# Optimization experiments

Measured on AMD Instinct MI355X. Metric: run time of the kernel, lower is better.

The kernel has to match this reference:

```python
import jax, jax.numpy as jnp
import numpy as np

B, T, I, H, L, O = 2048, 512, 1, 64, 2, 1


def _lstm_layer(x, Wih, Whh, b):
    """Single LSTM layer, batch_first x: [B, T, in] -> [B, T, H].
    PyTorch gate order: i, f, g, o. b = b_ih + b_hh (folded)."""
    Bn = x.shape[0]
    Hn = Whh.shape[1]
    # Precompute input contribution for all timesteps (hoisted out of scan)
    xg = jnp.einsum('bti,gi->btg', x, Wih) + b  # [B, T, 4H]

    def step(carry, xg_t):
        h, c = carry
        g = xg_t + h @ Whh.T  # [B, 4H]
        i, f, gg, o = jnp.split(g, 4, axis=-1)
        i = jax.nn.sigmoid(i)
        f = jax.nn.sigmoid(f)
        gg = jnp.tanh(gg)
        o = jax.nn.sigmoid(o)
        c = f * c + i * gg
        h = o * jnp.tanh(c)
        return (h, c), h

    h0 = jnp.zeros((Bn, Hn), x.dtype)
    c0 = jnp.zeros((Bn, Hn), x.dtype)
    (_, _), hs = jax.lax.scan(step, (h0, c0), jnp.swapaxes(xg, 0, 1))  # hs: [T, B, H]
    return jnp.swapaxes(hs, 0, 1)


def setup_inputs() -> dict:
    key = jax.random.key(0)
    ks = jax.random.split(key, 11)
    s = 1.0 / np.sqrt(H)  # torch default uniform bound
    u = lambda k, shp: jax.random.uniform(k, shp, jnp.float32, -s, s)
    return {
        'x': jax.random.normal(ks[0], (B, T, I), jnp.float32),
        'Wih0': u(ks[1], (4 * H, I)),
        'Whh0': u(ks[2], (4 * H, H)),
        'bih0': u(ks[3], (4 * H,)),
        'bhh0': u(ks[4], (4 * H,)),
        'Wih1': u(ks[5], (4 * H, H)),
        'Whh1': u(ks[6], (4 * H, H)),
        'bih1': u(ks[7], (4 * H,)),
        'bhh1': u(ks[8], (4 * H,)),
        'fcW': u(ks[9], (O, H)),
        'fcb': u(ks[10], (O,)),
    }


def reference(x, Wih0, Whh0, bih0, bhh0, Wih1, Whh1, bih1, bhh1, fcW, fcb):
    h1 = _lstm_layer(x, Wih0, Whh0, bih0 + bhh0)   # [B, T, H]
    h2 = _lstm_layer(h1, Wih1, Whh1, bih1 + bhh1)  # [B, T, H]
    return h2[:, -1, :] @ fcW.T + fcb               # [B, O]
```

## Files before the change

kernel.cpp:

```cpp
#include <hip/hip_runtime.h>


#define TT 512
#define HH 64
#define BT 8

typedef __attribute__((ext_vector_type(4))) int i32x4;

#define MFMAI8 __builtin_amdgcn_mfma_i32_16x16x64_i8

#define WSCALE 260096.0f
#define HSCALE 32512.0f
#define LOG2E  1.44269504f
constexpr float C_SIG = (float)(256.0 / (260096.0 * 32512.0) * 1.4426950408889634);
constexpr float C_TGH = (float)(2.0 * 256.0 / (260096.0 * 32512.0) * 1.4426950408889634);

__device__ __forceinline__ float exp2_hw(float x) {
    float r; asm("v_exp_f32 %0, %1" : "=v"(r) : "v"(x)); return r;
}
__device__ __forceinline__ float exp2n_hw(float x) {
    float r; asm("v_exp_f32 %0, -%1" : "=v"(r) : "v"(x)); return r;
}
__device__ __forceinline__ float gate4s(float p0, float p1, float p2, float p3, float& c) {
    float gi = __builtin_amdgcn_rcpf(1.f + exp2n_hw(p0));
    float gf = __builtin_amdgcn_rcpf(1.f + exp2n_hw(p1));
    float gg = 1.f - 2.f * __builtin_amdgcn_rcpf(1.f + exp2_hw(p2));
    float go = __builtin_amdgcn_rcpf(1.f + exp2n_hw(p3));
    c = fmaf(gf, c, gi * gg);
    float tc = 1.f - 2.f * __builtin_amdgcn_rcpf(1.f + exp2_hw(c * (2.f * LOG2E)));
    return go * tc;
}
__device__ __forceinline__ int dpp_ror8_i(int v) {
    return __builtin_amdgcn_update_dpp(v, v, 0x128, 0xF, 0xF, true);
}
__device__ __forceinline__ void cvtW16(const float* __restrict__ p, i32x4& hi, i32x4& lo) {
    #pragma unroll
    for (int r = 0; r < 4; ++r) {
        int hw = 0, lw = 0;
        #pragma unroll
        for (int b = 0; b < 4; ++b) {
            int wq = (int)rintf(p[4 * b + r] * WSCALE);
            int h8 = (wq + 128) >> 8;
            int l8 = wq - (h8 << 8);
            hw |= (h8 & 0xFF) << (8 * b);
            lw |= (l8 & 0xFF) << (8 * b);
        }
        hi[r] = hw; lo[r] = lw;
    }
}

__global__ __launch_bounds__(1024) void lstm_mfma(
    const float* __restrict__ x,
    const float* __restrict__ Wih0, const float* __restrict__ Whh0,
    const float* __restrict__ bih0, const float* __restrict__ bhh0,
    const float* __restrict__ Wih1, const float* __restrict__ Whh1,
    const float* __restrict__ bih1, const float* __restrict__ bhh1,
    const float* __restrict__ fcW, const float* __restrict__ fcb,
    float* __restrict__ out)
{
    __shared__ float xs[BT][TT + 1];
    __shared__ __align__(16) signed char aH[2][2][2][64][16];
    __shared__ float hF[BT][HH + 1];
    __shared__ float fcw_s[HH];

    const int t    = threadIdx.x;
    const int lane = t & 63;
    const int w    = t >> 6;
    const int b0   = blockIdx.x * BT;
    const int m    = lane & 15;
    const int q    = lane >> 4;
    const int ts   = m >> 3;
    const int bpk  = m & 7;
    const int jpk  = 4 * w + q;

    for (int i = t; i < BT * TT; i += 1024)
        xs[i >> 9][i & (TT - 1)] = x[(size_t)(b0 + (i >> 9)) * TT + (i & (TT - 1))];
    {
        int* z = (int*)aH;
        for (int i = t; i < 2048; i += 1024)
            z[i] = ((i >> 8) & 1) ? 0x80808080 : 0;
    }
    if (t < HH) fcw_s[t] = fcW[t];

    i32x4 A0h, A0l, I1h, I1l, H1h, H1l;
    {
        const int rho = (m & 3) * 64 + 4 * w + (m >> 2);
        cvtW16(Whh0 + rho * HH + q * 16, A0h, A0l);
        cvtW16(Wih1 + rho * HH + q * 16, I1h, I1l);
        cvtW16(Whh1 + rho * HH + q * 16, H1h, H1l);
    }

    i32x4 corrA, corrB;
    {
        i32x4 ones; ones[0] = 0x01010101; ones[1] = 0x01010101;
        ones[2] = 0x01010101; ones[3] = 0x01010101;
        i32x4 zz = {0, 0, 0, 0};
        i32x4 Sa = MFMAI8(A0h, ones, zz, 0, 0, 0);
        i32x4 Sb = MFMAI8(I1h, ones, zz, 0, 0, 0);
        Sb = MFMAI8(H1h, ones, Sb, 0, 0, 0);
        #pragma unroll
        for (int r = 0; r < 4; ++r) { corrA[r] = Sa[r] << 7; corrB[r] = Sb[r] << 7; }
    }

    float wxb[4], bia[4];
    #pragma unroll
    for (int v = 0; v < 4; ++v) {
        const int r = v * 64 + jpk;
        const float sc = (v == 2) ? 2.f * LOG2E : LOG2E;
        if (ts) { wxb[v] = 0.f;          bia[v] = (bih1[r] + bhh1[r]) * sc; }
        else    { wxb[v] = Wih0[r] * sc; bia[v] = (bih0[r] + bhh0[r]) * sc; }
    }
    const int wl = ((jpk >> 4) << 4) + bpk;
    const int wb = ((jpk & 3) << 2) | ((jpk >> 2) & 3);
    float c = 0.f;

    __syncthreads();

    #pragma unroll 2
    for (int k = 0; k < TT; ++k) {
        const int p = k & 1, pn = p ^ 1;
        i32x4 bh1 = *(const i32x4*)&aH[0][p][0][lane][0];
        i32x4 bl1 = *(const i32x4*)&aH[0][p][1][lane][0];
        i32x4 bh2 = *(const i32x4*)&aH[1][p][0][lane][0];
        i32x4 bl2 = *(const i32x4*)&aH[1][p][1][lane][0];
        i32x4 z4 = {0, 0, 0, 0};
        i32x4 aHHr = z4, bHHr = z4;
        i32x4 aMDr = corrA, bMDr = corrB;
        aHHr = MFMAI8(A0h, bh1, aHHr, 0, 0, 0);
        bHHr = MFMAI8(I1h, bh1, bHHr, 0, 0, 0);
        aMDr = MFMAI8(A0h, bl1, aMDr, 0, 0, 0);
        bMDr = MFMAI8(I1h, bl1, bMDr, 0, 0, 0);
        aMDr = MFMAI8(A0l, bh1, aMDr, 0, 0, 0);
        bMDr = MFMAI8(I1l, bh1, bMDr, 0, 0, 0);
        bHHr = MFMAI8(H1h, bh2, bHHr, 0, 0, 0);
        bMDr = MFMAI8(H1h, bl2, bMDr, 0, 0, 0);
        bMDr = MFMAI8(H1l, bh2, bMDr, 0, 0, 0);

        float xb = xs[bpk][k];
        float pre[4];
        #pragma unroll
        for (int r = 0; r < 4; ++r) {
            int hh = aHHr[r] + dpp_ror8_i(bHHr[r]);
            int md = aMDr[r] + dpp_ror8_i(bMDr[r]);
            float P = (float)((hh << 8) + md);
            const float Cr = (r == 2) ? C_TGH : C_SIG;
            pre[r] = fmaf(P, Cr, fmaf(wxb[r], xb, bia[r]));
        }
        float hv = gate4s(pre[0], pre[1], pre[2], pre[3], c);
        if (k == 0) {
            hv = ts ? 0.f : hv;
            c  = ts ? 0.f : c;
        }
        int hq = __float_as_int(fmaf(hv, HSCALE, 12582912.f)) - 0x4B400000;
        aH[ts][pn][0][wl][wb] = (signed char)(hq >> 8);
        aH[ts][pn][1][wl][wb] = (signed char)(hq ^ 0x80);
        __syncthreads();
    }

    {
        i32x4 bh1 = *(const i32x4*)&aH[0][0][0][lane][0];
        i32x4 bl1 = *(const i32x4*)&aH[0][0][1][lane][0];
        i32x4 bh2 = *(const i32x4*)&aH[1][0][0][lane][0];
        i32x4 bl2 = *(const i32x4*)&aH[1][0][1][lane][0];
        i32x4 z4 = {0, 0, 0, 0};
        i32x4 bHHr = z4, bMDr = corrB;
        bHHr = MFMAI8(I1h, bh1, bHHr, 0, 0, 0);
        bMDr = MFMAI8(I1h, bl1, bMDr, 0, 0, 0);
        bMDr = MFMAI8(I1l, bh1, bMDr, 0, 0, 0);
        bHHr = MFMAI8(H1h, bh2, bHHr, 0, 0, 0);
        bMDr = MFMAI8(H1h, bl2, bMDr, 0, 0, 0);
        bMDr = MFMAI8(H1l, bh2, bMDr, 0, 0, 0);
        float pre[4];
        #pragma unroll
        for (int r = 0; r < 4; ++r) {
            int hh = dpp_ror8_i(bHHr[r]);
            int md = dpp_ror8_i(bMDr[r]);
            float P = (float)((hh << 8) + md);
            const float Cr = (r == 2) ? C_TGH : C_SIG;
            pre[r] = fmaf(P, Cr, bia[r]);
        }
        float hv = gate4s(pre[0], pre[1], pre[2], pre[3], c);
        if (ts) hF[bpk][jpk] = hv;
    }
    __syncthreads();

    if (t < BT) {
        float s = fcb[0];
        #pragma unroll 8
        for (int j = 0; j < HH; ++j)
            s = fmaf(hF[t][j], fcw_s[j], s);
        out[b0 + t] = s;
    }
}

extern "C" void kernel_launch(void* const* d_in, const int* in_sizes, int n_in,
                              void* d_out, int out_size, void* d_ws, size_t ws_size,
                              hipStream_t stream) {
    const float* x    = (const float*)d_in[0];
    const float* Wih0 = (const float*)d_in[1];
    const float* Whh0 = (const float*)d_in[2];
    const float* bih0 = (const float*)d_in[3];
    const float* bhh0 = (const float*)d_in[4];
    const float* Wih1 = (const float*)d_in[5];
    const float* Whh1 = (const float*)d_in[6];
    const float* bih1 = (const float*)d_in[7];
    const float* bhh1 = (const float*)d_in[8];
    const float* fcW  = (const float*)d_in[9];
    const float* fcb  = (const float*)d_in[10];
    float* out = (float*)d_out;

    lstm_mfma<<<dim3(2048 / BT), dim3(1024), 0, stream>>>(
        x, Wih0, Whh0, bih0, bhh0, Wih1, Whh1, bih1, bhh1, fcW, fcb, out);
}
```

Baseline: 433.9 us.

## Halve block size, have each wave compute both layers for two hidden-unit groups

Blocks shrink from 1024 to 512 threads, and each wave now owns two 4-row weight groups per layer, so it holds twice the int8 weight fragments and issues twice the MFMAs. Each lane computes both the layer-1 and layer-2 gates instead of splitting layers across lane halves. The first timestep is peeled so the per-step k==0 special case is gone. Sched barriers separate the MFMA phase from the two gate phases. The intent is fewer threads in each block barrier and two resident blocks per CU, at the cost of more VGPR pressure and more serial work per wave.

Result: faster. 419.3 us, median of 2 (-3.4%).

```diff
diff --git a/kernel.cpp b/kernel.cpp
--- a/kernel.cpp
+++ b/kernel.cpp
@@ -49,7 +49,7 @@
     }
 }
 
-__global__ __launch_bounds__(1024) void lstm_mfma(
+__global__ __launch_bounds__(512, 2) void lstm_mfma(
     const float* __restrict__ x,
     const float* __restrict__ Wih0, const float* __restrict__ Whh0,
     const float* __restrict__ bih0, const float* __restrict__ bhh0,
@@ -65,95 +65,150 @@
 
     const int t    = threadIdx.x;
     const int lane = t & 63;
-    const int w    = t >> 6;
+    const int v    = t >> 6;
     const int b0   = blockIdx.x * BT;
     const int m    = lane & 15;
     const int q    = lane >> 4;
     const int ts   = m >> 3;
     const int bpk  = m & 7;
-    const int jpk  = 4 * w + q;
-
-    for (int i = t; i < BT * TT; i += 1024)
+    const int j    = 4 * (2 * v + ts) + q;
+
+    for (int i = t; i < BT * TT; i += 512)
         xs[i >> 9][i & (TT - 1)] = x[(size_t)(b0 + (i >> 9)) * TT + (i & (TT - 1))];
     {
         int* z = (int*)aH;
-        for (int i = t; i < 2048; i += 1024)
+        for (int i = t; i < 2048; i += 512)
             z[i] = ((i >> 8) & 1) ? 0x80808080 : 0;
     }
     if (t < HH) fcw_s[t] = fcW[t];
 
-    i32x4 A0h, A0l, I1h, I1l, H1h, H1l;
-    {
-        const int rho = (m & 3) * 64 + 4 * w + (m >> 2);
-        cvtW16(Whh0 + rho * HH + q * 16, A0h, A0l);
-        cvtW16(Wih1 + rho * HH + q * 16, I1h, I1l);
-        cvtW16(Whh1 + rho * HH + q * 16, H1h, H1l);
-    }
-
-    i32x4 corrA, corrB;
+    i32x4 A0h[2], A0l[2], I1h[2], I1l[2], H1h[2], H1l[2];
+    #pragma unroll
+    for (int i = 0; i < 2; ++i) {
+        const int rho = (m & 3) * 64 + 4 * (2 * v + i) + (m >> 2);
+        cvtW16(Whh0 + rho * HH + q * 16, A0h[i], A0l[i]);
+        cvtW16(Wih1 + rho * HH + q * 16, I1h[i], I1l[i]);
+        cvtW16(Whh1 + rho * HH + q * 16, H1h[i], H1l[i]);
+    }
+
+    i32x4 corrA[2], corrB[2];
     {
         i32x4 ones; ones[0] = 0x01010101; ones[1] = 0x01010101;
         ones[2] = 0x01010101; ones[3] = 0x01010101;
         i32x4 zz = {0, 0, 0, 0};
-        i32x4 Sa = MFMAI8(A0h, ones, zz, 0, 0, 0);
-        i32x4 Sb = MFMAI8(I1h, ones, zz, 0, 0, 0);
-        Sb = MFMAI8(H1h, ones, Sb, 0, 0, 0);
-        #pragma unroll
-        for (int r = 0; r < 4; ++r) { corrA[r] = Sa[r] << 7; corrB[r] = Sb[r] << 7; }
-    }
-
-    float wxb[4], bia[4];
+        #pragma unroll
+        for (int i = 0; i < 2; ++i) {
+            i32x4 Sa = MFMAI8(A0h[i], ones, zz, 0, 0, 0);
+            i32x4 Sb = MFMAI8(H1h[i], ones, MFMAI8(I1h[i], ones, zz, 0, 0, 0), 0, 0, 0);
+            #pragma unroll
+            for (int r = 0; r < 4; ++r) {
+                corrA[i][r] = Sa[r] << 7;
+                corrB[i][r] = Sb[r] << 7;
+            }
+        }
+    }
+
+    float wxb[4], bia1[4], bia2[4];
     #pragma unroll
-    for (int v = 0; v < 4; ++v) {
-        const int r = v * 64 + jpk;
-        const float sc = (v == 2) ? 2.f * LOG2E : LOG2E;
-        if (ts) { wxb[v] = 0.f;          bia[v] = (bih1[r] + bhh1[r]) * sc; }
-        else    { wxb[v] = Wih0[r] * sc; bia[v] = (bih0[r] + bhh0[r]) * sc; }
-    }
-    const int wl = ((jpk >> 4) << 4) + bpk;
-    const int wb = ((jpk & 3) << 2) | ((jpk >> 2) & 3);
-    float c = 0.f;
+    for (int g = 0; g < 4; ++g) {
+        const int r = g * 64 + j;
+        const float sc = (g == 2) ? 2.f * LOG2E : LOG2E;
+        wxb[g]  = Wih0[r] * sc;
+        bia1[g] = (bih0[r] + bhh0[r]) * sc;
+        bia2[g] = (bih1[r] + bhh1[r]) * sc;
+    }
+    const int wl = ((j >> 4) << 4) + bpk;
+    const int wb = ((j & 3) << 2) | ((j >> 2) & 3);
+    float c1 = 0.f, c2 = 0.f;
 
     __syncthreads();
 
+    {
+        i32x4 bh1 = *(const i32x4*)&aH[0][0][0][lane][0];
+        i32x4 bl1 = *(const i32x4*)&aH[0][0][1][lane][0];
+        i32x4 aHH[2], aMD[2];
+        #pragma unroll
+        for (int i = 0; i < 2; ++i) {
+            i32x4 z4 = {0, 0, 0, 0};
+            aHH[i] = MFMAI8(A0h[i], bh1, z4, 0, 0, 0);
+            aMD[i] = MFMAI8(A0l[i], bh1, MFMAI8(A0h[i], bl1, corrA[i], 0, 0, 0), 0, 0, 0);
+        }
+        float xb = xs[bpk][0];
+        float pre[4];
+        #pragma unroll
+        for (int r = 0; r < 4; ++r) {
+            int Pa = (aHH[0][r] << 8) + aMD[0][r];
+            int Pb = (aHH[1][r] << 8) + aMD[1][r];
+            int P  = Pa + dpp_ror8_i(Pb);
+            const float Cr = (r == 2) ? C_TGH : C_SIG;
+            pre[r] = fmaf((float)P, Cr, fmaf(wxb[r], xb, bia1[r]));
+        }
+        float h1v = gate4s(pre[0], pre[1], pre[2], pre[3], c1);
+        int hq = __float_as_int(fmaf(h1v, HSCALE, 12582912.f)) - 0x4B400000;
+        aH[0][1][0][wl][wb] = (signed char)(hq >> 8);
+        aH[0][1][1][wl][wb] = (signed char)(hq ^ 0x80);
+        __syncthreads();
+    }
+
     #pragma unroll 2
-    for (int k = 0; k < TT; ++k) {
+    for (int k = 1; k < TT; ++k) {
         const int p = k & 1, pn = p ^ 1;
         i32x4 bh1 = *(const i32x4*)&aH[0][p][0][lane][0];
         i32x4 bl1 = *(const i32x4*)&aH[0][p][1][lane][0];
         i32x4 bh2 = *(const i32x4*)&aH[1][p][0][lane][0];
         i32x4 bl2 = *(const i32x4*)&aH[1][p][1][lane][0];
-        i32x4 z4 = {0, 0, 0, 0};
-        i32x4 aHHr = z4, bHHr = z4;
-        i32x4 aMDr = corrA, bMDr = corrB;
-        aHHr = MFMAI8(A0h, bh1, aHHr, 0, 0, 0);
-        bHHr = MFMAI8(I1h, bh1, bHHr, 0, 0, 0);
-        aMDr = MFMAI8(A0h, bl1, aMDr, 0, 0, 0);
-        bMDr = MFMAI8(I1h, bl1, bMDr, 0, 0, 0);
-        aMDr = MFMAI8(A0l, bh1, aMDr, 0, 0, 0);
-        bMDr = MFMAI8(I1l, bh1, bMDr, 0, 0, 0);
-        bHHr = MFMAI8(H1h, bh2, bHHr, 0, 0, 0);
-        bMDr = MFMAI8(H1h, bl2, bMDr, 0, 0, 0);
-        bMDr = MFMAI8(H1l, bh2, bMDr, 0, 0, 0);
-
         float xb = xs[bpk][k];
-        float pre[4];
-        #pragma unroll
-        for (int r = 0; r < 4; ++r) {
-            int hh = aHHr[r] + dpp_ror8_i(bHHr[r]);
-            int md = aMDr[r] + dpp_ror8_i(bMDr[r]);
-            float P = (float)((hh << 8) + md);
-            const float Cr = (r == 2) ? C_TGH : C_SIG;
-            pre[r] = fmaf(P, Cr, fmaf(wxb[r], xb, bia[r]));
-        }
-        float hv = gate4s(pre[0], pre[1], pre[2], pre[3], c);
-        if (k == 0) {
-            hv = ts ? 0.f : hv;
-            c  = ts ? 0.f : c;
-        }
-        int hq = __float_as_int(fmaf(hv, HSCALE, 12582912.f)) - 0x4B400000;
-        aH[ts][pn][0][wl][wb] = (signed char)(hq >> 8);
-        aH[ts][pn][1][wl][wb] = (signed char)(hq ^ 0x80);
+
+        i32x4 aHH[2], aMD[2], bHH[2], bMD[2];
+        #pragma unroll
+        for (int i = 0; i < 2; ++i) {
+            i32x4 z4 = {0, 0, 0, 0};
+            aHH[i] = MFMAI8(A0h[i], bh1, z4, 0, 0, 0);
+            aMD[i] = MFMAI8(A0l[i], bh1, MFMAI8(A0h[i], bl1, corrA[i], 0, 0, 0), 0, 0, 0);
+        }
+        #pragma unroll
+        for (int i = 0; i < 2; ++i) {
+            i32x4 z4 = {0, 0, 0, 0};
+            bHH[i] = MFMAI8(H1h[i], bh2, MFMAI8(I1h[i], bh1, z4, 0, 0, 0), 0, 0, 0);
+            bMD[i] = MFMAI8(H1l[i], bh2,
+                     MFMAI8(H1h[i], bl2,
+                     MFMAI8(I1l[i], bh1,
+                     MFMAI8(I1h[i], bl1, corrB[i], 0, 0, 0), 0, 0, 0), 0, 0, 0), 0, 0, 0);
+        }
+        __builtin_amdgcn_sched_barrier(0);
+
+        {
+            float pre[4];
+            #pragma unroll
+            for (int r = 0; r < 4; ++r) {
+                int Pa = (aHH[0][r] << 8) + aMD[0][r];
+                int Pb = (aHH[1][r] << 8) + aMD[1][r];
+                int P  = Pa + dpp_ror8_i(Pb);
+                const float Cr = (r == 2) ? C_TGH : C_SIG;
+                pre[r] = fmaf((float)P, Cr, fmaf(wxb[r], xb, bia1[r]));
+            }
+            float h1v = gate4s(pre[0], pre[1], pre[2], pre[3], c1);
+            int hq = __float_as_int(fmaf(h1v, HSCALE, 12582912.f)) - 0x4B400000;
+            aH[0][pn][0][wl][wb] = (signed char)(hq >> 8);
+            aH[0][pn][1][wl][wb] = (signed char)(hq ^ 0x80);
+        }
+        __builtin_amdgcn_sched_barrier(0);
+
+        {
+            float pre[4];
+            #pragma unroll
+            for (int r = 0; r < 4; ++r) {
+                int Pc = (bHH[0][r] << 8) + bMD[0][r];
+                int Pd = (bHH[1][r] << 8) + bMD[1][r];
+                int P  = Pc + dpp_ror8_i(Pd);
+                const float Cr = (r == 2) ? C_TGH : C_SIG;
+                pre[r] = fmaf((float)P, Cr, bia2[r]);
+            }
+            float h2v = gate4s(pre[0], pre[1], pre[2], pre[3], c2);
+            int hq = __float_as_int(fmaf(h2v, HSCALE, 12582912.f)) - 0x4B400000;
+            aH[1][pn][0][wl][wb] = (signed char)(hq >> 8);
+            aH[1][pn][1][wl][wb] = (signed char)(hq ^ 0x80);
+        }
         __syncthreads();
     }
 
@@ -162,33 +217,35 @@
         i32x4 bl1 = *(const i32x4*)&aH[0][0][1][lane][0];
         i32x4 bh2 = *(const i32x4*)&aH[1][0][0][lane][0];
         i32x4 bl2 = *(const i32x4*)&aH[1][0][1][lane][0];
-        i32x4 z4 = {0, 0, 0, 0};
-        i32x4 bHHr = z4, bMDr = corrB;
-        bHHr = MFMAI8(I1h, bh1, bHHr, 0, 0, 0);
-        bMDr = MFMAI8(I1h, bl1, bMDr, 0, 0, 0);
-        bMDr = MFMAI8(I1l, bh1, bMDr, 0, 0, 0);
-        bHHr = MFMAI8(H1h, bh2, bHHr, 0, 0, 0);
-        bMDr = MFMAI8(H1h, bl2, bMDr, 0, 0, 0);
-        bMDr = MFMAI8(H1l, bh2, bMDr, 0, 0, 0);
+        i32x4 bHH[2], bMD[2];
+        #pragma unroll
+        for (int i = 0; i < 2; ++i) {
+            i32x4 z4 = {0, 0, 0, 0};
+            bHH[i] = MFMAI8(H1h[i], bh2, MFMAI8(I1h[i], bh1, z4, 0, 0, 0), 0, 0, 0);
+            bMD[i] = MFMAI8(H1l[i], bh2,
+                     MFMAI8(H1h[i], bl2,
+                     MFMAI8(I1l[i], bh1,
+                     MFMAI8(I1h[i], bl1, corrB[i], 0, 0, 0), 0, 0, 0), 0, 0, 0), 0, 0, 0);
+        }
         float pre[4];
         #pragma unroll
         for (int r = 0; r < 4; ++r) {
-            int hh = dpp_ror8_i(bHHr[r]);
-            int md = dpp_ror8_i(bMDr[r]);
-            float P = (float)((hh << 8) + md);
+            int Pc = (bHH[0][r] << 8) + bMD[0][r];
+            int Pd = (bHH[1][r] << 8) + bMD[1][r];
+            int P  = Pc + dpp_ror8_i(Pd);
             const float Cr = (r == 2) ? C_TGH : C_SIG;
-            pre[r] = fmaf(P, Cr, bia[r]);
-        }
-        float hv = gate4s(pre[0], pre[1], pre[2], pre[3], c);
-        if (ts) hF[bpk][jpk] = hv;
+            pre[r] = fmaf((float)P, Cr, bia2[r]);
+        }
+        float h2v = gate4s(pre[0], pre[1], pre[2], pre[3], c2);
+        hF[bpk][j] = h2v;
     }
     __syncthreads();
 
     if (t < BT) {
         float s = fcb[0];
         #pragma unroll 8
-        for (int j = 0; j < HH; ++j)
-            s = fmaf(hF[t][j], fcw_s[j], s);
+        for (int jj = 0; jj < HH; ++jj)
+            s = fmaf(hF[t][jj], fcw_s[jj], s);
         out[b0 + t] = s;
     }
 }
@@ -209,6 +266,6 @@
     const float* fcb  = (const float*)d_in[10];
     float* out = (float*)d_out;
 
-    lstm_mfma<<<dim3(2048 / BT), dim3(1024), 0, stream>>>(
+    lstm_mfma<<<dim3(2048 / BT), dim3(512), 0, stream>>>(
         x, Wih0, Whh0, bih0, bhh0, Wih1, Whh1, bih1, bhh1, fcW, fcb, out);
 }
```
